# Performance work log

Measured on AMD Instinct MI355X. Metric: run time of the kernel, lower is better.

## Reference

```python
import jax, jax.numpy as jnp
import numpy as np

# geomloss SamplesLoss(loss='sinkhorn', p=2, blur=0.05, scaling=0.8) constants
P = 2
BLUR = 0.05
SCALING = 0.8
# inputs are L2-normalized, so the point-cloud diameter is bounded by 2
DIAMETER = 2.0


def _eps_list():
    # geomloss epsilon_schedule: anneal eps from diameter**p down to blur**p
    e = [DIAMETER ** P]
    e += [float(np.exp(v)) for v in np.arange(P * np.log(DIAMETER), P * np.log(BLUR), P * np.log(SCALING))]
    e += [BLUR ** P]
    return e


def _cost(a, b):
    # geomloss p=2 cost: 0.5 * squared Euclidean distance, shape [N, M]
    sq = jnp.sum(a * a, -1)[:, None] + jnp.sum(b * b, -1)[None, :] - 2.0 * (a @ b.T)
    return 0.5 * jnp.maximum(sq, 0.0)


def _softmin(eps, C, h):
    # h = log-weights + potential/eps over the reduced axis; returns [N]
    return -eps * jax.nn.logsumexp(h[None, :] - C / eps, axis=1)


def _sinkhorn_divergence(x, y):
    # Debiased Sinkhorn divergence with epsilon-scaling (geomloss sinkhorn_tensorized)
    sg = jax.lax.stop_gradient
    N, M = x.shape[0], y.shape[0]
    a_log = jnp.full((N,), -np.log(N), x.dtype)  # uniform weights 1/N (log)
    b_log = jnp.full((M,), -np.log(M), y.dtype)

    C_xy = _cost(x, y)
    C_yx = C_xy.T
    C_xx = _cost(x, x)
    C_yy = _cost(y, y)
    # Sinkhorn loop runs without gradient (envelope theorem), like torch no_grad
    D_xy, D_yx, D_xx, D_yy = sg(C_xy), sg(C_yx), sg(C_xx), sg(C_yy)

    eps_list = _eps_list()
    eps = eps_list[0]
    g_ab = _softmin(eps, D_yx, a_log)   # potential on y for OT(a, b)
    f_ba = _softmin(eps, D_xy, b_log)   # potential on x for OT(a, b)
    f_aa = _softmin(eps, D_xx, a_log)   # debiasing potential OT(a, a)
    g_bb = _softmin(eps, D_yy, b_log)   # debiasing potential OT(b, b)

    for eps in eps_list:
        ft_ba = _softmin(eps, D_xy, b_log + g_ab / eps)
        gt_ab = _softmin(eps, D_yx, a_log + f_ba / eps)
        ft_aa = _softmin(eps, D_xx, a_log + f_aa / eps)
        gt_bb = _softmin(eps, D_yy, b_log + g_bb / eps)
        f_ba = 0.5 * (f_ba + ft_ba)
        g_ab = 0.5 * (g_ab + gt_ab)
        f_aa = 0.5 * (f_aa + ft_aa)
        g_bb = 0.5 * (g_bb + gt_bb)

    # final extrapolation with gradients enabled, dual potentials detached
    eps = eps_list[-1]
    f_ba, g_ab = (
        _softmin(eps, C_xy, sg(b_log + g_ab / eps)),
        _softmin(eps, C_yx, sg(a_log + f_ba / eps)),
    )
    f_aa = _softmin(eps, C_xx, sg(a_log + f_aa / eps))
    g_bb = _softmin(eps, C_yy, sg(b_log + g_bb / eps))

    # S_eps(a,b) = <a, f_ba - f_aa> + <b, g_ab - g_bb>, uniform weights
    return jnp.mean(f_ba - f_aa) + jnp.mean(g_ab - g_bb)


def setup_inputs() -> dict:
    key = jax.random.key(0)
    kx, ky = jax.random.split(key)
    x = jax.random.normal(kx, (4096, 64), jnp.float32)
    y = jax.random.normal(ky, (4096, 64), jnp.float32)
    return {"x": x, "y": y}


def reference(x, y):
    x = x / jnp.linalg.norm(x, axis=1, keepdims=True)
    y = y / jnp.linalg.norm(y, axis=1, keepdims=True)
    return _sinkhorn_divergence(x, y)
```

## Files before the change

kernel.cpp:

```cpp
#include <hip/hip_runtime.h>
#include <math.h>

#define NPTS 4096
#define DIM 64
#define LOGW2 (-12.0f)
#define NEGINF (-__builtin_inff())

typedef __bf16 bf16x8 __attribute__((ext_vector_type(8)));
typedef float f32x4 __attribute__((ext_vector_type(4)));

static __device__ __forceinline__ f32x4 mfma16(bf16x8 a, bf16x8 b, f32x4 c) {
  return __builtin_amdgcn_mfma_f32_16x16x32_bf16(a, b, c, 0, 0, 0);
}
static __device__ __forceinline__ float exp2v(float x) {
  return __builtin_amdgcn_exp2f(x);
}
static __device__ __forceinline__ float log2v(float x) {
  return __builtin_amdgcn_logf(x);
}

__global__ __launch_bounds__(256) void norm_repack_kernel(
    const float* __restrict__ x, const float* __restrict__ y,
    __bf16* __restrict__ xhf, __bf16* __restrict__ xlf,
    __bf16* __restrict__ yhf, __bf16* __restrict__ ylf) {
  __shared__ float tf[32][72];
  int r0 = blockIdx.x * 32;
  const float* src;
  __bf16 *dh, *dl;
  int rbase;
  if (r0 < NPTS) { src = x; dh = xhf; dl = xlf; rbase = r0; }
  else           { src = y; dh = yhf; dl = ylf; rbase = r0 - NPTS; }

  int wave = threadIdx.x >> 6, lane = threadIdx.x & 63;
  #pragma unroll
  for (int i = 0; i < 8; ++i) {
    int wrow = wave * 8 + i;
    float v = src[(size_t)(rbase + wrow) * DIM + lane];
    float s = v * v;
    #pragma unroll
    for (int o = 32; o; o >>= 1) s += __shfl_xor(s, o, 64);
    tf[wrow][lane] = v * (1.0f / sqrtf(s));
  }
  __syncthreads();

  int tt   = threadIdx.x >> 7;
  int idx  = threadIdx.x & 127;
  int c    = idx >> 6, L = idx & 63;
  int quad = L >> 4, mrow = L & 15;
  const float* rp = &tf[tt * 16 + mrow][c * 32 + quad * 8];
  bf16x8 hv, lv;
  #pragma unroll
  for (int j = 0; j < 8; ++j) {
    float v = rp[j];
    __bf16 h = (__bf16)v;
    hv[j] = h;
    lv[j] = (__bf16)(v - (float)h);
  }
  size_t ob = (size_t)(rbase / 16 + tt) * 1024 + c * 512 + L * 8;
  *(bf16x8*)(dh + ob) = hv;
  *(bf16x8*)(dl + ob) = lv;
}

__global__ __launch_bounds__(512, 4) void fused_pass_kernel(
    const __bf16* __restrict__ xhf, const __bf16* __restrict__ xlf,
    const __bf16* __restrict__ yhf, const __bf16* __restrict__ ylf,
    const float* __restrict__ potOld, float* __restrict__ potNew,
    float inv_eps2, float epsl2, int use_pot, int avg) {
  __shared__ float hlds[NPTS];
  __shared__ float mred[8][32];
  __shared__ float sred[8][32];

  int mat = blockIdx.x >> 7;
  int rb  = blockIdx.x & 127;
  const __bf16 *Ah, *Al, *Bh, *Bl;
  if (mat == 0)      { Ah = xhf; Al = xlf; Bh = yhf; Bl = ylf; }
  else if (mat == 1) { Ah = yhf; Al = ylf; Bh = xhf; Bl = xlf; }
  else if (mat == 2) { Ah = xhf; Al = xlf; Bh = xhf; Bl = xlf; }
  else               { Ah = yhf; Al = ylf; Bh = yhf; Bl = ylf; }
  int ridx = (mat == 0) ? 1 : ((mat == 1) ? 0 : mat);
  const float* pot = potOld + (size_t)ridx * NPTS;

  {
    int j8 = threadIdx.x * 8;
    float4 p0, p1;
    if (use_pot) {
      float4 q0 = *(const float4*)(pot + j8);
      float4 q1 = *(const float4*)(pot + j8 + 4);
      p0.x = fmaf(q0.x, inv_eps2, LOGW2); p0.y = fmaf(q0.y, inv_eps2, LOGW2);
      p0.z = fmaf(q0.z, inv_eps2, LOGW2); p0.w = fmaf(q0.w, inv_eps2, LOGW2);
      p1.x = fmaf(q1.x, inv_eps2, LOGW2); p1.y = fmaf(q1.y, inv_eps2, LOGW2);
      p1.z = fmaf(q1.z, inv_eps2, LOGW2); p1.w = fmaf(q1.w, inv_eps2, LOGW2);
    } else {
      p0.x = p0.y = p0.z = p0.w = LOGW2;
      p1 = p0;
    }
    *(float4*)(hlds + j8) = p0;
    *(float4*)(hlds + j8 + 4) = p1;
  }
  __syncthreads();

  int wave = threadIdx.x >> 6, L = threadIdx.x & 63;
  int mrow = L & 15, quad = L >> 4;
  int lofs = L * 8;
  int i0 = rb * 32;

  bf16x8 Ah0[2], Ah1[2], Al0[2], Al1[2];
  #pragma unroll
  for (int rs = 0; rs < 2; ++rs) {
    size_t ab = (size_t)(rb * 2 + rs) * 1024 + lofs;
    Ah0[rs] = *(const bf16x8*)(Ah + ab);
    Ah1[rs] = *(const bf16x8*)(Ah + ab + 512);
    Al0[rs] = *(const bf16x8*)(Al + ab);
    Al1[rs] = *(const bf16x8*)(Al + ab + 512);
  }

  float sm[8], ss[8];
  #pragma unroll
  for (int i = 0; i < 8; ++i) { sm[i] = NEGINF; ss[i] = 0.0f; }

  size_t jt0 = (size_t)(wave * 32) * 1024 + lofs;
  int hb0 = wave * 512;

  #pragma unroll 1
  for (int tp = 0; tp < 16; ++tp) {
    size_t o0 = jt0 + (size_t)tp * 2048;
    bf16x8 b0h0 = *(const bf16x8*)(Bh + o0);
    bf16x8 b0h1 = *(const bf16x8*)(Bh + o0 + 512);
    bf16x8 b0l0 = *(const bf16x8*)(Bl + o0);
    bf16x8 b0l1 = *(const bf16x8*)(Bl + o0 + 512);
    bf16x8 b1h0 = *(const bf16x8*)(Bh + o0 + 1024);
    bf16x8 b1h1 = *(const bf16x8*)(Bh + o0 + 1536);
    bf16x8 b1l0 = *(const bf16x8*)(Bl + o0 + 1024);
    bf16x8 b1l1 = *(const bf16x8*)(Bl + o0 + 1536);
    float hp0 = hlds[hb0 + tp * 32 + mrow] - inv_eps2;
    float hp1 = hlds[hb0 + tp * 32 + 16 + mrow] - inv_eps2;

    #pragma unroll
    for (int rs = 0; rs < 2; ++rs) {
      f32x4 acc0 = {0.0f, 0.0f, 0.0f, 0.0f};
      acc0 = mfma16(Ah0[rs], b0h0, acc0);
      acc0 = mfma16(Ah1[rs], b0h1, acc0);
      acc0 = mfma16(Al0[rs], b0h0, acc0);
      acc0 = mfma16(Al1[rs], b0h1, acc0);
      acc0 = mfma16(Ah0[rs], b0l0, acc0);
      acc0 = mfma16(Ah1[rs], b0l1, acc0);
      f32x4 acc1 = {0.0f, 0.0f, 0.0f, 0.0f};
      acc1 = mfma16(Ah0[rs], b1h0, acc1);
      acc1 = mfma16(Ah1[rs], b1h1, acc1);
      acc1 = mfma16(Al0[rs], b1h0, acc1);
      acc1 = mfma16(Al1[rs], b1h1, acc1);
      acc1 = mfma16(Ah0[rs], b1l0, acc1);
      acc1 = mfma16(Ah1[rs], b1l1, acc1);
      #pragma unroll
      for (int q = 0; q < 4; ++q) {
        int id = rs * 4 + q;
        float tv0 = fmaf(fminf(acc0[q], 1.0f), inv_eps2, hp0);
        float tv1 = fmaf(fminf(acc1[q], 1.0f), inv_eps2, hp1);
        float mn = fmaxf(sm[id], fmaxf(tv0, tv1));
        ss[id] = fmaf(ss[id], exp2v(sm[id] - mn),
                      exp2v(tv0 - mn) + exp2v(tv1 - mn));
        sm[id] = mn;
      }
    }
  }

  #pragma unroll
  for (int o = 1; o < 16; o <<= 1) {
    #pragma unroll
    for (int i = 0; i < 8; ++i) {
      float m2 = __shfl_xor(sm[i], o, 64);
      float s2 = __shfl_xor(ss[i], o, 64);
      float mn = fmaxf(sm[i], m2);
      ss[i] = ss[i] * exp2v(sm[i] - mn) + s2 * exp2v(m2 - mn);
      sm[i] = mn;
    }
  }

  if (mrow == 0) {
    #pragma unroll
    for (int rs = 0; rs < 2; ++rs)
      #pragma unroll
      for (int q = 0; q < 4; ++q) {
        int row = rs * 16 + quad * 4 + q;
        mred[wave][row] = sm[rs * 4 + q];
        sred[wave][row] = ss[rs * 4 + q];
      }
  }
  __syncthreads();

  if (threadIdx.x < 32) {
    int row = threadIdx.x;
    float m = mred[0][row], s = sred[0][row];
    #pragma unroll
    for (int w = 1; w < 8; ++w) {
      float m2 = mred[w][row], s2 = sred[w][row];
      float mn = fmaxf(m, m2);
      s = s * exp2v(m - mn) + s2 * exp2v(m2 - mn);
      m = mn;
    }
    float ft = -epsl2 * (m + log2v(s));
    float v = avg ? 0.5f * (potOld[(size_t)mat * NPTS + i0 + row] + ft) : ft;
    potNew[(size_t)mat * NPTS + i0 + row] = v;
  }
}

__global__ __launch_bounds__(256) void final_kernel(
    const float* __restrict__ pot, float* __restrict__ out) {
  __shared__ float red[256];
  float s = 0.0f;
  for (int j = threadIdx.x; j < NPTS; j += 256)
    s += (pot[j] - pot[2 * NPTS + j]) + (pot[NPTS + j] - pot[3 * NPTS + j]);
  red[threadIdx.x] = s;
  __syncthreads();
  #pragma unroll
  for (int o = 128; o; o >>= 1) {
    if (threadIdx.x < o) red[threadIdx.x] += red[threadIdx.x + o];
    __syncthreads();
  }
  if (threadIdx.x == 0) out[0] = red[0] / (float)NPTS;
}

extern "C" void kernel_launch(void* const* d_in, const int* in_sizes, int n_in,
                              void* d_out, int out_size, void* d_ws, size_t ws_size,
                              hipStream_t stream) {
  const float* x = (const float*)d_in[0];
  const float* y = (const float*)d_in[1];
  char* ws = (char*)d_ws;

  __bf16* xhf = (__bf16*)ws;
  __bf16* xlf = xhf + (size_t)NPTS * DIM;
  __bf16* yhf = xlf + (size_t)NPTS * DIM;
  __bf16* ylf = yhf + (size_t)NPTS * DIM;
  float* potA = (float*)(ylf + (size_t)NPTS * DIM);
  float* potB = potA + 4 * (size_t)NPTS;
  size_t needed = (size_t)((char*)(potB + 4 * (size_t)NPTS) - ws);
  if (ws_size < needed) return;

  norm_repack_kernel<<<256, 256, 0, stream>>>(x, y, xhf, xlf, yhf, ylf);

  double lst[32];
  int c = 0;
  lst[c++] = 4.0;
  double start = 2.0 * log(2.0), stop = 2.0 * log(0.05), step = 2.0 * log(0.8);
  for (int k = 0;; ++k) {
    double v = start + (double)k * step;
    if (v <= stop) break;
    lst[c++] = exp(v);
  }
  lst[c++] = 0.05 * 0.05;

  const double LOG2E = 1.4426950408889634074;
  const double LN2   = 0.6931471805599453094;

  for (int p = 0; p < c + 2; ++p) {
    double e = (p == 0) ? lst[0] : ((p <= c) ? lst[p - 1] : lst[c - 1]);
    float inv_eps2 = (float)(LOG2E / e);
    float epsl2    = (float)(e * LN2);
    int use_pot = (p > 0) ? 1 : 0;
    int avg = (p >= 1 && p <= c) ? 1 : 0;
    const float* po = (p & 1) ? potB : potA;
    float* pn       = (p & 1) ? potA : potB;
    fused_pass_kernel<<<512, 512, 0, stream>>>(xhf, xlf, yhf, ylf, po, pn,
                                               inv_eps2, epsl2, use_pot, avg);
  }
  final_kernel<<<1, 256, 0, stream>>>(potB, (float*)d_out);
}
```

Measured before the change: 787.0 us.

## Double row tile per block to 64 rows and prefetch next column tile

Each block now handles 64 rows instead of 32, so every loaded B column tile feeds twice as many MFMA row sub-tiles, and the grid shrinks from 512 to 256 blocks. The column-tile loads are software-pipelined by loading tile tp+1 into registers while tile tp is computed. This raises register pressure (launch bounds relaxed to 2 blocks per SM), and 256 blocks may underfill the 256 CUs of the device, reducing occupancy and latency hiding.

```diff
diff --git a/kernel.cpp b/kernel.cpp
--- a/kernel.cpp
+++ b/kernel.cpp
@@ -61,17 +61,17 @@
   *(bf16x8*)(dl + ob) = lv;
 }
 
-__global__ __launch_bounds__(512, 4) void fused_pass_kernel(
+__global__ __launch_bounds__(512, 2) void fused_pass_kernel(
     const __bf16* __restrict__ xhf, const __bf16* __restrict__ xlf,
     const __bf16* __restrict__ yhf, const __bf16* __restrict__ ylf,
     const float* __restrict__ potOld, float* __restrict__ potNew,
     float inv_eps2, float epsl2, int use_pot, int avg) {
   __shared__ float hlds[NPTS];
-  __shared__ float mred[8][32];
-  __shared__ float sred[8][32];
-
-  int mat = blockIdx.x >> 7;
-  int rb  = blockIdx.x & 127;
+  __shared__ float mred[8][64];
+  __shared__ float sred[8][64];
+
+  int mat = blockIdx.x >> 6;
+  int rb  = blockIdx.x & 63;
   const __bf16 *Ah, *Al, *Bh, *Bl;
   if (mat == 0)      { Ah = xhf; Al = xlf; Bh = yhf; Bl = ylf; }
   else if (mat == 1) { Ah = yhf; Al = ylf; Bh = xhf; Bl = xlf; }
@@ -102,55 +102,65 @@
   int wave = threadIdx.x >> 6, L = threadIdx.x & 63;
   int mrow = L & 15, quad = L >> 4;
   int lofs = L * 8;
-  int i0 = rb * 32;
-
-  bf16x8 Ah0[2], Ah1[2], Al0[2], Al1[2];
-  #pragma unroll
-  for (int rs = 0; rs < 2; ++rs) {
-    size_t ab = (size_t)(rb * 2 + rs) * 1024 + lofs;
+  int i0 = rb * 64;
+
+  bf16x8 Ah0[4], Ah1[4], Al0[4], Al1[4];
+  #pragma unroll
+  for (int rs = 0; rs < 4; ++rs) {
+    size_t ab = (size_t)(rb * 4 + rs) * 1024 + lofs;
     Ah0[rs] = *(const bf16x8*)(Ah + ab);
     Ah1[rs] = *(const bf16x8*)(Ah + ab + 512);
     Al0[rs] = *(const bf16x8*)(Al + ab);
     Al1[rs] = *(const bf16x8*)(Al + ab + 512);
   }
 
-  float sm[8], ss[8];
-  #pragma unroll
-  for (int i = 0; i < 8; ++i) { sm[i] = NEGINF; ss[i] = 0.0f; }
+  float sm[16], ss[16];
+  #pragma unroll
+  for (int i = 0; i < 16; ++i) { sm[i] = NEGINF; ss[i] = 0.0f; }
 
   size_t jt0 = (size_t)(wave * 32) * 1024 + lofs;
   int hb0 = wave * 512;
 
+  bf16x8 c0h0 = *(const bf16x8*)(Bh + jt0);
+  bf16x8 c0h1 = *(const bf16x8*)(Bh + jt0 + 512);
+  bf16x8 c0l0 = *(const bf16x8*)(Bl + jt0);
+  bf16x8 c0l1 = *(const bf16x8*)(Bl + jt0 + 512);
+  bf16x8 c1h0 = *(const bf16x8*)(Bh + jt0 + 1024);
+  bf16x8 c1h1 = *(const bf16x8*)(Bh + jt0 + 1536);
+  bf16x8 c1l0 = *(const bf16x8*)(Bl + jt0 + 1024);
+  bf16x8 c1l1 = *(const bf16x8*)(Bl + jt0 + 1536);
+
   #pragma unroll 1
   for (int tp = 0; tp < 16; ++tp) {
-    size_t o0 = jt0 + (size_t)tp * 2048;
-    bf16x8 b0h0 = *(const bf16x8*)(Bh + o0);
-    bf16x8 b0h1 = *(const bf16x8*)(Bh + o0 + 512);
-    bf16x8 b0l0 = *(const bf16x8*)(Bl + o0);
-    bf16x8 b0l1 = *(const bf16x8*)(Bl + o0 + 512);
-    bf16x8 b1h0 = *(const bf16x8*)(Bh + o0 + 1024);
-    bf16x8 b1h1 = *(const bf16x8*)(Bh + o0 + 1536);
-    bf16x8 b1l0 = *(const bf16x8*)(Bl + o0 + 1024);
-    bf16x8 b1l1 = *(const bf16x8*)(Bl + o0 + 1536);
+    int tpn = (tp < 15) ? tp + 1 : 15;
+    size_t on = jt0 + (size_t)tpn * 2048;
+    bf16x8 n0h0 = *(const bf16x8*)(Bh + on);
+    bf16x8 n0h1 = *(const bf16x8*)(Bh + on + 512);
+    bf16x8 n0l0 = *(const bf16x8*)(Bl + on);
+    bf16x8 n0l1 = *(const bf16x8*)(Bl + on + 512);
+    bf16x8 n1h0 = *(const bf16x8*)(Bh + on + 1024);
+    bf16x8 n1h1 = *(const bf16x8*)(Bh + on + 1536);
+    bf16x8 n1l0 = *(const bf16x8*)(Bl + on + 1024);
+    bf16x8 n1l1 = *(const bf16x8*)(Bl + on + 1536);
     float hp0 = hlds[hb0 + tp * 32 + mrow] - inv_eps2;
     float hp1 = hlds[hb0 + tp * 32 + 16 + mrow] - inv_eps2;
 
     #pragma unroll
-    for (int rs = 0; rs < 2; ++rs) {
+    for (int rs = 0; rs < 4; ++rs) {
       f32x4 acc0 = {0.0f, 0.0f, 0.0f, 0.0f};
-      acc0 = mfma16(Ah0[rs], b0h0, acc0);
-      acc0 = mfma16(Ah1[rs], b0h1, acc0);
-      acc0 = mfma16(Al0[rs], b0h0, acc0);
-      acc0 = mfma16(Al1[rs], b0h1, acc0);
-      acc0 = mfma16(Ah0[rs], b0l0, acc0);
-      acc0 = mfma16(Ah1[rs], b0l1, acc0);
+      acc0 = mfma16(Ah0[rs], c0h0, acc0);
+      acc0 = mfma16(Ah1[rs], c0h1, acc0);
+      acc0 = mfma16(Al0[rs], c0h0, acc0);
+      acc0 = mfma16(Al1[rs], c0h1, acc0);
+      acc0 = mfma16(Ah0[rs], c0l0, acc0);
+      acc0 = mfma16(Ah1[rs], c0l1, acc0);
       f32x4 acc1 = {0.0f, 0.0f, 0.0f, 0.0f};
-      acc1 = mfma16(Ah0[rs], b1h0, acc1);
-      acc1 = mfma16(Ah1[rs], b1h1, acc1);
-      acc1 = mfma16(Al0[rs], b1h0, acc1);
-      acc1 = mfma16(Al1[rs], b1h1, acc1);
-      acc1 = mfma16(Ah0[rs], b1l0, acc1);
-      acc1 = mfma16(Ah1[rs], b1l1, acc1);
+      acc1 = mfma16(Ah0[rs], c1h0, acc1);
+      acc1 = mfma16(Ah1[rs], c1h1, acc1);
+      acc1 = mfma16(Al0[rs], c1h0, acc1);
+      acc1 = mfma16(Al1[rs], c1h1, acc1);
+      acc1 = mfma16(Ah0[rs], c1l0, acc1);
+      acc1 = mfma16(Ah1[rs], c1l1, acc1);
       #pragma unroll
       for (int q = 0; q < 4; ++q) {
         int id = rs * 4 + q;
@@ -162,12 +172,14 @@
         sm[id] = mn;
       }
     }
+    c0h0 = n0h0; c0h1 = n0h1; c0l0 = n0l0; c0l1 = n0l1;
+    c1h0 = n1h0; c1h1 = n1h1; c1l0 = n1l0; c1l1 = n1l1;
   }
 
   #pragma unroll
   for (int o = 1; o < 16; o <<= 1) {
     #pragma unroll
-    for (int i = 0; i < 8; ++i) {
+    for (int i = 0; i < 16; ++i) {
       float m2 = __shfl_xor(sm[i], o, 64);
       float s2 = __shfl_xor(ss[i], o, 64);
       float mn = fmaxf(sm[i], m2);
@@ -178,7 +190,7 @@
 
   if (mrow == 0) {
     #pragma unroll
-    for (int rs = 0; rs < 2; ++rs)
+    for (int rs = 0; rs < 4; ++rs)
       #pragma unroll
       for (int q = 0; q < 4; ++q) {
         int row = rs * 16 + quad * 4 + q;
@@ -188,7 +200,7 @@
   }
   __syncthreads();
 
-  if (threadIdx.x < 32) {
+  if (threadIdx.x < 64) {
     int row = threadIdx.x;
     float m = mred[0][row], s = sred[0][row];
     #pragma unroll
@@ -260,7 +272,7 @@
     int avg = (p >= 1 && p <= c) ? 1 : 0;
     const float* po = (p & 1) ? potB : potA;
     float* pn       = (p & 1) ? potA : potB;
-    fused_pass_kernel<<<512, 512, 0, stream>>>(xhf, xlf, yhf, ylf, po, pn,
+    fused_pass_kernel<<<256, 512, 0, stream>>>(xhf, xlf, yhf, ylf, po, pn,
                                                inv_eps2, epsl2, use_pot, avg);
   }
   final_kernel<<<1, 256, 0, stream>>>(potB, (float*)d_out);
```

Measured after the change: 772.0 us. About the same (-1.9%).
